# Kernel tuning notes

Measured on AMD Instinct MI355X. Metric: run time of the kernel, lower is better.

Reference implementation:

```python
import jax, jax.numpy as jnp
import numpy as np

N = 100000      # nodes
E = 1600000     # directed edges
F_IN = 128      # node feature dim
H = 128         # hidden dim
C = 16          # classes


def setup_inputs() -> dict:
    key = jax.random.key(0)
    ks = jax.random.split(key, 8)
    s = 1.0 / np.sqrt(H)
    return {
        "x": jax.random.normal(ks[0], (N, F_IN), dtype=jnp.float32),
        "edge_index": jax.random.randint(ks[1], (2, E), 0, N, dtype=jnp.int32),
        "W1": jax.random.normal(ks[2], (F_IN, H), dtype=jnp.float32) * s,
        "b1": jnp.zeros((H,), jnp.float32),
        "W2": jax.random.normal(ks[3], (H, H), dtype=jnp.float32) * s,
        "b2": jnp.zeros((H,), jnp.float32),
        "W3": jax.random.normal(ks[4], (H, H), dtype=jnp.float32) * s,
        "b3": jnp.zeros((H,), jnp.float32),
        "Wfc": jax.random.normal(ks[5], (H, C), dtype=jnp.float32) * s,
        "bfc": jnp.zeros((C,), jnp.float32),
    }


def _gcn_conv(x, W, b, src, dst, norm):
    # x' = b + scatter_add over edges of norm * (x @ W)[src] into dst
    h = x @ W                                   # [N, H] dense GEMM
    msg = h[src] * norm[:, None]                # [E+N, H] gather + scale
    out = jax.ops.segment_sum(msg, dst, num_segments=N)  # scatter-add
    return out + b


def reference(x, edge_index, W1, b1, W2, b2, W3, b3, Wfc, bfc):
    loops = jnp.arange(N, dtype=edge_index.dtype)
    src = jnp.concatenate([edge_index[0], loops])   # [E+N] with self-loops
    dst = jnp.concatenate([edge_index[1], loops])
    # symmetric normalization deg^{-1/2}[src] * deg^{-1/2}[dst] (PyG default)
    deg = jax.ops.segment_sum(jnp.ones_like(dst, dtype=x.dtype), dst, num_segments=N)
    dinv = jax.lax.rsqrt(deg)                       # deg >= 1 due to self-loops
    norm = dinv[src] * dinv[dst]

    h = jax.nn.elu(_gcn_conv(x, W1, b1, src, dst, norm))   # dropout is identity in eval
    h = jax.nn.elu(_gcn_conv(h, W2, b2, src, dst, norm))
    h = jax.nn.elu(_gcn_conv(h, W3, b3, src, dst, norm))
    logits = h @ Wfc + bfc                                  # [N, C]
    return jax.nn.log_softmax(logits, axis=-1)
```

## Files before the change

### kernel.cpp

```cpp
#include <hip/hip_runtime.h>
#include <math.h>

#define HDIM 128
#define CDIM 16
#define CAP 48
#define ASTR 136
#define NBINS 256
#define TILE 4096
#define F2SPLIT 4

typedef unsigned short u16;
typedef unsigned int u32;
typedef __attribute__((ext_vector_type(8))) short short8;
typedef __attribute__((ext_vector_type(4))) float f32x4;
typedef __attribute__((ext_vector_type(2))) float f32x2;

__device__ inline u16 f2bf(float f) {
  u32 u = __float_as_uint(f);
  u += 0x7fffu + ((u >> 16) & 1u);
  return (u16)(u >> 16);
}
__device__ inline float bf_lo(u32 p) { return __uint_as_float(p << 16); }
__device__ inline float bf_hi(u32 p) { return __uint_as_float(p & 0xffff0000u); }
__device__ inline u32 pack2(float a, float b) {
  return (u32)f2bf(a) | ((u32)f2bf(b) << 16);
}

__device__ inline void acc_word(f32x2& acc, u32 w) {
  f32x2 x;
  x.x = __uint_as_float(w << 16);
  x.y = __uint_as_float(w & 0xffff0000u);
  asm("v_pk_add_f32 %0, %1, %2" : "=v"(acc) : "v"(x), "v"(acc));
}
__device__ inline f32x2 xor16_add(f32x2 a) {
  f32x2 o;
  o.x = __shfl_xor(a.x, 16, 32);
  o.y = __shfl_xor(a.y, 16, 32);
  asm("v_pk_add_f32 %0, %1, %2" : "=v"(a) : "v"(o), "v"(a));
  return a;
}


__global__ __launch_bounds__(256) void bin_kernel(const int* __restrict__ ei,
                                                  int* __restrict__ cursor,
                                                  int2* __restrict__ bins,
                                                  int binCap, int E, int npb, int nbE,
                                                  int* __restrict__ deg, int N,
                                                  const float* __restrict__ W0,
                                                  const float* __restrict__ W1,
                                                  const float* __restrict__ W2,
                                                  u16* __restrict__ Wt) {
  int tid = threadIdx.x;
  if (blockIdx.x >= nbE) {
    int t = (blockIdx.x - nbE) * 256 + tid;
    int which = t >> 14, idx = t & 16383;
    int n = idx >> 7, k = idx & 127;
    const float* W = which == 0 ? W0 : (which == 1 ? W1 : W2);
    Wt[(size_t)which * HDIM * HDIM + n * HDIM + k] = f2bf(W[k * HDIM + n]);
    return;
  }
  {
    int i = blockIdx.x * 256 + tid;
    if (i < N) deg[i] = 0;
  }
  __shared__ int2 eds[TILE];
  __shared__ int base[NBINS], rank[NBINS], hist[NBINS];
  int t0 = blockIdx.x * TILE;
  int n = min(TILE, E - t0);
  for (int i = tid; i < NBINS; i += 256) { hist[i] = 0; rank[i] = 0; }
  __syncthreads();
  for (int i = tid; i < n; i += 256) {
    int s = ei[t0 + i];
    int d = ei[E + t0 + i];
    eds[i] = make_int2(d, s);
    atomicAdd(&hist[d / npb], 1);
  }
  __syncthreads();
  for (int i = tid; i < NBINS; i += 256) {
    int h = hist[i];
    base[i] = h ? atomicAdd(&cursor[i], h) : 0;
  }
  __syncthreads();
  for (int i = tid; i < n; i += 256) {
    int2 e = eds[i];
    int b = e.x / npb;
    int r = base[b] + atomicAdd(&rank[b], 1);
    if (r < binCap) bins[(size_t)b * binCap + r] = e;
  }
}

__global__ __launch_bounds__(256) void fill2_kernel(const int2* __restrict__ bins,
                                                    const int* __restrict__ cursor,
                                                    int binCap, int* __restrict__ deg,
                                                    int* __restrict__ csr) {
  int b = blockIdx.x & (NBINS - 1);
  int part = blockIdx.x >> 8;
  int cnt = min(cursor[b], binCap);
  const int2* eb = bins + (size_t)b * binCap;
  for (int i = part * 256 + threadIdx.x; i < cnt; i += 256 * F2SPLIT) {
    int2 e = eb[i];
    int p = atomicAdd(&deg[e.x], 1);
    if (p < CAP) csr[(size_t)e.x * CAP + p] = e.y;
  }
}

__global__ __launch_bounds__(256) void pad_kernel(const int* __restrict__ deg,
                                                  int* __restrict__ csr, int N) {
  int n = blockIdx.x * 256 + threadIdx.x;
  if (n >= N) return;
  int d = min(deg[n], CAP);
  int dp = (d + 15) & ~15;
  int* row = csr + (size_t)n * CAP;
  for (int i = d; i < dp; ++i) row[i] = N;
}


template <bool FP32IN>
__global__ __launch_bounds__(256) void gemm_k(const void* __restrict__ Xv,
                                              const u16* __restrict__ Wt,
                                              const int* __restrict__ deg,
                                              u16* __restrict__ G, int N) {
  __shared__ u16 As[64 * ASTR];
  __shared__ u16 Wsm[128 * ASTR];
  int tid = threadIdx.x;
  int row0 = blockIdx.x * 64;

  {
    int r = tid >> 2, c = tid & 3;
    int rg = row0 + r;
    if (rg >= N) rg = N - 1;
    uint4* dst = (uint4*)(As + r * ASTR + c * 32);
    if (FP32IN) {
      const float4* src = (const float4*)((const float*)Xv + (size_t)rg * HDIM + c * 32);
#pragma unroll
      for (int j = 0; j < 4; ++j) {
        float4 a = src[2 * j], b = src[2 * j + 1];
        uint4 o;
        o.x = pack2(a.x, a.y); o.y = pack2(a.z, a.w);
        o.z = pack2(b.x, b.y); o.w = pack2(b.z, b.w);
        dst[j] = o;
      }
    } else {
      const uint4* src = (const uint4*)((const u16*)Xv + (size_t)rg * HDIM + c * 32);
      dst[0] = src[0]; dst[1] = src[1]; dst[2] = src[2]; dst[3] = src[3];
    }
  }
  {
    int r = tid >> 1, h = tid & 1;
    const uint4* src = (const uint4*)(Wt + r * HDIM + h * 64);
    uint4* dst = (uint4*)(Wsm + r * ASTR + h * 64);
#pragma unroll
    for (int i = 0; i < 8; ++i) dst[i] = src[i];
  }
  __syncthreads();

  int w = tid >> 6;
  int l = tid & 63;
  int m = l & 15, q = l >> 4;

  f32x4 acc[8];
#pragma unroll
  for (int i = 0; i < 8; ++i) acc[i] = (f32x4){0.f, 0.f, 0.f, 0.f};

#pragma unroll
  for (int kc = 0; kc < 4; ++kc) {
    short8 af = *(const short8*)(As + (w * 16 + m) * ASTR + kc * 32 + q * 8);
#pragma unroll
    for (int nt = 0; nt < 8; ++nt) {
      short8 bfr = *(const short8*)(Wsm + (nt * 16 + m) * ASTR + kc * 32 + q * 8);
      acc[nt] = __builtin_amdgcn_mfma_f32_16x16x32_bf16(af, bfr, acc[nt], 0, 0, 0);
    }
  }
  __syncthreads();

  float dv[4];
#pragma unroll
  for (int r = 0; r < 4; ++r) {
    int rg = row0 + w * 16 + q * 4 + r;
    dv[r] = rsqrtf((float)(deg[rg < N ? rg : N - 1] + 1));
  }
#pragma unroll
  for (int nt = 0; nt < 8; ++nt)
#pragma unroll
    for (int r = 0; r < 4; ++r)
      As[(w * 16 + q * 4 + r) * ASTR + nt * 16 + m] = f2bf(acc[nt][r] * dv[r]);
  __syncthreads();

  {
    int r = tid >> 2, c = tid & 3;
    int rg = row0 + r;
    if (rg < N) {
      uint4* dst = (uint4*)(G + (size_t)rg * HDIM + c * 32);
      const uint4* src = (const uint4*)(As + r * ASTR + c * 32);
      dst[0] = src[0]; dst[1] = src[1]; dst[2] = src[2]; dst[3] = src[3];
    }
  }
}


__device__ inline void gather32(const u16* __restrict__ G, const int* __restrict__ deg,
                                const int* __restrict__ csr,
                                const float4* __restrict__ b4, int node, int cl, float* v) {
  const char* Gb = (const char*)G;
  int l = cl & 15, g = cl >> 4;
  uint4 sr = make_uint4(0, 0, 0, 0);
  if (g == 0) sr = *(const uint4*)(Gb + ((size_t)node << 8) + (l << 4));
  f32x2 p0, p1, p2, p3;
  p0.x = bf_lo(sr.x); p0.y = bf_hi(sr.x);
  p1.x = bf_lo(sr.y); p1.y = bf_hi(sr.y);
  p2.x = bf_lo(sr.z); p2.y = bf_hi(sr.z);
  p3.x = bf_lo(sr.w); p3.y = bf_hi(sr.w);

  int dfull = deg[node];
  int d = min(dfull, CAP);
  int dp = (d + 15) & ~15;
  const int* row = csr + (size_t)node * CAP;
  int i0 = row[cl];
  int i1 = (cl < 16) ? row[32 + cl] : 0;

#define GLD(u) (*(const uint4*)(Gb + (((u32)(u)) << 8) + (l << 4)))
#define AW(gv) { acc_word(p0, gv.x); acc_word(p1, gv.y); acc_word(p2, gv.z); acc_word(p3, gv.w); }
  for (int k = 0; k < dp; k += 16) {
    int s = k < 32 ? i0 : i1;
    int bl = (k < 32 ? k : 0) + g;
    int u0 = __shfl(s, bl + 0, 32), u1 = __shfl(s, bl + 2, 32);
    int u2 = __shfl(s, bl + 4, 32), u3 = __shfl(s, bl + 6, 32);
    int u4 = __shfl(s, bl + 8, 32), u5 = __shfl(s, bl + 10, 32);
    int u6 = __shfl(s, bl + 12, 32), u7 = __shfl(s, bl + 14, 32);
    uint4 g0 = GLD(u0), g1 = GLD(u1), g2 = GLD(u2), g3 = GLD(u3);
    uint4 g4 = GLD(u4), g5 = GLD(u5), g6 = GLD(u6), g7 = GLD(u7);
    AW(g0) AW(g1) AW(g2) AW(g3) AW(g4) AW(g5) AW(g6) AW(g7)
  }
#undef AW
#undef GLD
  p0 = xor16_add(p0); p1 = xor16_add(p1);
  p2 = xor16_add(p2); p3 = xor16_add(p3);

  float dvn = rsqrtf((float)(dfull + 1));
  float4 b0 = b4[l * 2], b1 = b4[l * 2 + 1];
  v[0] = fmaf(dvn, p0.x, b0.x); v[1] = fmaf(dvn, p0.y, b0.y);
  v[2] = fmaf(dvn, p1.x, b0.z); v[3] = fmaf(dvn, p1.y, b0.w);
  v[4] = fmaf(dvn, p2.x, b1.x); v[5] = fmaf(dvn, p2.y, b1.y);
  v[6] = fmaf(dvn, p3.x, b1.z); v[7] = fmaf(dvn, p3.y, b1.w);
#pragma unroll
  for (int j = 0; j < 8; ++j) v[j] = v[j] > 0.f ? v[j] : expm1f(v[j]);
}


__global__ __launch_bounds__(256) void agg_bf(const u16* __restrict__ G,
                                              const int* __restrict__ deg,
                                              const int* __restrict__ csr,
                                              const float* __restrict__ b,
                                              u16* __restrict__ out, int N) {
  int node = blockIdx.x * 8 + (threadIdx.x >> 5);
  if (node >= N) return;
  int cl = threadIdx.x & 31;
  float v[8];
  gather32(G, deg, csr, (const float4*)b, node, cl, v);
  if (cl < 16) {
    uint4 o;
    o.x = pack2(v[0], v[1]); o.y = pack2(v[2], v[3]);
    o.z = pack2(v[4], v[5]); o.w = pack2(v[6], v[7]);
    *(uint4*)(out + (size_t)node * HDIM + cl * 8) = o;
  }
}


__global__ __launch_bounds__(256) void agg_fc(const u16* __restrict__ G,
                                              const int* __restrict__ deg,
                                              const int* __restrict__ csr,
                                              const float* __restrict__ b,
                                              const float* __restrict__ Wfc,
                                              const float* __restrict__ bfc,
                                              float* __restrict__ out, int N) {
  __shared__ u16 As[8 * ASTR];
  __shared__ float Wl[HDIM * CDIM];
  int tid = threadIdx.x;
  for (int i = tid; i < HDIM * CDIM; i += 256) Wl[i] = Wfc[i];

  int node0 = blockIdx.x * 8;
  int nr = tid >> 5, cl = tid & 31, l = cl & 15;
  int node = node0 + nr;
  if (node < N) {
    float v[8];
    gather32(G, deg, csr, (const float4*)b, node, cl, v);
    if (cl < 16) {
      uint4 o;
      o.x = pack2(v[0], v[1]); o.y = pack2(v[2], v[3]);
      o.z = pack2(v[4], v[5]); o.w = pack2(v[6], v[7]);
      *(uint4*)(As + nr * ASTR + l * 8) = o;
    }
  }
  __syncthreads();

  int lr = tid >> 4, c = tid & 15;
  if (lr >= 8) return;
  int rg = node0 + lr;
  if (rg >= N) return;
  const u16* hrow = As + lr * ASTR;
  float acc = bfc[c];
#pragma unroll 4
  for (int k8 = 0; k8 < 16; ++k8) {
    uint4 g = *(const uint4*)(hrow + k8 * 8);
    const float* wk = Wl + (k8 * 8) * CDIM + c;
    acc = fmaf(bf_lo(g.x), wk[0 * CDIM], acc);
    acc = fmaf(bf_hi(g.x), wk[1 * CDIM], acc);
    acc = fmaf(bf_lo(g.y), wk[2 * CDIM], acc);
    acc = fmaf(bf_hi(g.y), wk[3 * CDIM], acc);
    acc = fmaf(bf_lo(g.z), wk[4 * CDIM], acc);
    acc = fmaf(bf_hi(g.z), wk[5 * CDIM], acc);
    acc = fmaf(bf_lo(g.w), wk[6 * CDIM], acc);
    acc = fmaf(bf_hi(g.w), wk[7 * CDIM], acc);
  }
  float mx = acc;
  for (int off = 8; off >= 1; off >>= 1) mx = fmaxf(mx, __shfl_xor(mx, off, 16));
  float ex = expf(acc - mx);
  float ssum = ex;
  for (int off = 8; off >= 1; off >>= 1) ssum += __shfl_xor(ssum, off, 16);
  out[(size_t)rg * CDIM + c] = (acc - mx) - logf(ssum);
}


extern "C" void kernel_launch(void* const* d_in, const int* in_sizes, int n_in,
                              void* d_out, int out_size, void* d_ws, size_t ws_size,
                              hipStream_t stream) {
  const float* x   = (const float*)d_in[0];
  const int*   ei  = (const int*)d_in[1];
  const float* W1  = (const float*)d_in[2];
  const float* b1  = (const float*)d_in[3];
  const float* W2  = (const float*)d_in[4];
  const float* b2  = (const float*)d_in[5];
  const float* W3  = (const float*)d_in[6];
  const float* b3  = (const float*)d_in[7];
  const float* Wfc = (const float*)d_in[8];
  const float* bfc = (const float*)d_in[9];

  const int N = in_sizes[0] / HDIM;
  const int E = in_sizes[1] / 2;
  const int npb = (N + NBINS - 1) / NBINS;
  const int binCap = (E + NBINS - 1) / NBINS + 1024;
  const int nbE = (E + TILE - 1) / TILE;
  const int nbW = 3 * HDIM * HDIM / 256;

  char* ws = (char*)d_ws;
  size_t off = 0;
  auto alloc = [&](size_t bytes) -> void* {
    void* p = ws + off;
    off += (bytes + 511) & ~(size_t)511;
    return p;
  };
  int*   deg    = (int*)alloc((size_t)N * 4);
  int*   cursor = (int*)alloc((size_t)NBINS * 4);
  int*   csr    = (int*)alloc((size_t)N * CAP * 4);
  int2*  bins   = (int2*)alloc((size_t)NBINS * binCap * 8);
  u16*   Wt     = (u16*)alloc((size_t)3 * HDIM * HDIM * 2);
  u16*   A      = (u16*)alloc((size_t)(N + 1) * HDIM * 2);
  u16*   B      = (u16*)alloc((size_t)(N + 1) * HDIM * 2);

  hipMemsetAsync(cursor, 0, (size_t)NBINS * 4, stream);
  hipMemsetAsync(A + (size_t)N * HDIM, 0, HDIM * 2, stream);
  hipMemsetAsync(B + (size_t)N * HDIM, 0, HDIM * 2, stream);
  bin_kernel<<<nbE + nbW, 256, 0, stream>>>(ei, cursor, bins, binCap, E, npb, nbE, deg, N, W1,
                                            W2, W3, Wt);
  fill2_kernel<<<NBINS * F2SPLIT, 256, 0, stream>>>(bins, cursor, binCap, deg, csr);
  pad_kernel<<<(N + 255) / 256, 256, 0, stream>>>(deg, csr, N);

  int grid64 = (N + 63) / 64;
  int grid8 = (N + 7) / 8;
  gemm_k<true><<<grid64, 256, 0, stream>>>(x, Wt, deg, A, N);
  agg_bf<<<grid8, 256, 0, stream>>>(A, deg, csr, b1, B, N);
  gemm_k<false><<<grid64, 256, 0, stream>>>(B, Wt + HDIM * HDIM, deg, A, N);
  agg_bf<<<grid8, 256, 0, stream>>>(A, deg, csr, b2, B, N);
  gemm_k<false><<<grid64, 256, 0, stream>>>(B, Wt + 2 * HDIM * HDIM, deg, A, N);
  agg_fc<<<grid8, 256, 0, stream>>>(A, deg, csr, b3, Wfc, bfc, (float*)d_out, N);
}
```

Measured before the change: 411.4 us.

## Aggregate each node with 16 lanes instead of 32 and drop cross-half reduction

The neighbour gather now assigns 16 lanes per node instead of 32 (two half-groups). Each lane walks all neighbours in steps of 8 with padding to multiples of 8, which removes the xor-shuffle reduction and the idle half-wave on writes. Other changes: 16 nodes per block, a hardware bf16 pack instruction, fast exp/log intrinsics, and the final FC reading fp32 hidden values from shared memory. Each lane now carries a longer serial dependent chain of loads per node, which may reduce memory-level parallelism per node, though more nodes are in flight per wave.

```diff
diff --git a/kernel.cpp b/kernel.cpp
--- a/kernel.cpp
+++ b/kernel.cpp
@@ -5,6 +5,7 @@
 #define CDIM 16
 #define CAP 48
 #define ASTR 136
+#define HSTR 132
 #define NBINS 256
 #define TILE 4096
 #define F2SPLIT 4
@@ -25,19 +26,16 @@
 __device__ inline u32 pack2(float a, float b) {
   return (u32)f2bf(a) | ((u32)f2bf(b) << 16);
 }
-
+__device__ inline u32 cvtpk(float a, float b) {
+  u32 r;
+  asm("v_cvt_pk_bf16_f32 %0, %1, %2" : "=v"(r) : "v"(a), "v"(b));
+  return r;
+}
 __device__ inline void acc_word(f32x2& acc, u32 w) {
   f32x2 x;
   x.x = __uint_as_float(w << 16);
   x.y = __uint_as_float(w & 0xffff0000u);
   asm("v_pk_add_f32 %0, %1, %2" : "=v"(acc) : "v"(x), "v"(acc));
-}
-__device__ inline f32x2 xor16_add(f32x2 a) {
-  f32x2 o;
-  o.x = __shfl_xor(a.x, 16, 32);
-  o.y = __shfl_xor(a.y, 16, 32);
-  asm("v_pk_add_f32 %0, %1, %2" : "=v"(a) : "v"(o), "v"(a));
-  return a;
 }
 
 
@@ -109,7 +107,7 @@
   int n = blockIdx.x * 256 + threadIdx.x;
   if (n >= N) return;
   int d = min(deg[n], CAP);
-  int dp = (d + 15) & ~15;
+  int dp = (d + 7) & ~7;
   int* row = csr + (size_t)n * CAP;
   for (int i = d; i < dp; ++i) row[i] = N;
 }
@@ -198,44 +196,41 @@
 }
 
 
-__device__ inline void gather32(const u16* __restrict__ G, const int* __restrict__ deg,
+__device__ inline void gather16(const u16* __restrict__ G, const int* __restrict__ deg,
                                 const int* __restrict__ csr,
-                                const float4* __restrict__ b4, int node, int cl, float* v) {
+                                const float4* __restrict__ b4, int node, int l, float* v) {
   const char* Gb = (const char*)G;
-  int l = cl & 15, g = cl >> 4;
-  uint4 sr = make_uint4(0, 0, 0, 0);
-  if (g == 0) sr = *(const uint4*)(Gb + ((size_t)node << 8) + (l << 4));
   f32x2 p0, p1, p2, p3;
-  p0.x = bf_lo(sr.x); p0.y = bf_hi(sr.x);
-  p1.x = bf_lo(sr.y); p1.y = bf_hi(sr.y);
-  p2.x = bf_lo(sr.z); p2.y = bf_hi(sr.z);
-  p3.x = bf_lo(sr.w); p3.y = bf_hi(sr.w);
-
+  {
+    uint4 sr = *(const uint4*)(Gb + ((size_t)node << 8) + (l << 4));
+    p0.x = bf_lo(sr.x); p0.y = bf_hi(sr.x);
+    p1.x = bf_lo(sr.y); p1.y = bf_hi(sr.y);
+    p2.x = bf_lo(sr.z); p2.y = bf_hi(sr.z);
+    p3.x = bf_lo(sr.w); p3.y = bf_hi(sr.w);
+  }
   int dfull = deg[node];
   int d = min(dfull, CAP);
-  int dp = (d + 15) & ~15;
+  int dp = (d + 7) & ~7;
   const int* row = csr + (size_t)node * CAP;
-  int i0 = row[cl];
-  int i1 = (cl < 16) ? row[32 + cl] : 0;
+  int i0 = row[l];
+  int i1 = d > 16 ? row[16 + l] : 0;
+  int i2 = d > 32 ? row[32 + l] : 0;
 
 #define GLD(u) (*(const uint4*)(Gb + (((u32)(u)) << 8) + (l << 4)))
 #define AW(gv) { acc_word(p0, gv.x); acc_word(p1, gv.y); acc_word(p2, gv.z); acc_word(p3, gv.w); }
-  for (int k = 0; k < dp; k += 16) {
-    int s = k < 32 ? i0 : i1;
-    int bl = (k < 32 ? k : 0) + g;
-    int u0 = __shfl(s, bl + 0, 32), u1 = __shfl(s, bl + 2, 32);
-    int u2 = __shfl(s, bl + 4, 32), u3 = __shfl(s, bl + 6, 32);
-    int u4 = __shfl(s, bl + 8, 32), u5 = __shfl(s, bl + 10, 32);
-    int u6 = __shfl(s, bl + 12, 32), u7 = __shfl(s, bl + 14, 32);
+  for (int k = 0; k < dp; k += 8) {
+    int s = k < 16 ? i0 : (k < 32 ? i1 : i2);
+    int bl = k & 15;
+    int u0 = __shfl(s, bl + 0, 16), u1 = __shfl(s, bl + 1, 16);
+    int u2 = __shfl(s, bl + 2, 16), u3 = __shfl(s, bl + 3, 16);
+    int u4 = __shfl(s, bl + 4, 16), u5 = __shfl(s, bl + 5, 16);
+    int u6 = __shfl(s, bl + 6, 16), u7 = __shfl(s, bl + 7, 16);
     uint4 g0 = GLD(u0), g1 = GLD(u1), g2 = GLD(u2), g3 = GLD(u3);
     uint4 g4 = GLD(u4), g5 = GLD(u5), g6 = GLD(u6), g7 = GLD(u7);
     AW(g0) AW(g1) AW(g2) AW(g3) AW(g4) AW(g5) AW(g6) AW(g7)
   }
 #undef AW
 #undef GLD
-  p0 = xor16_add(p0); p1 = xor16_add(p1);
-  p2 = xor16_add(p2); p3 = xor16_add(p3);
-
   float dvn = rsqrtf((float)(dfull + 1));
   float4 b0 = b4[l * 2], b1 = b4[l * 2 + 1];
   v[0] = fmaf(dvn, p0.x, b0.x); v[1] = fmaf(dvn, p0.y, b0.y);
@@ -243,7 +238,7 @@
   v[4] = fmaf(dvn, p2.x, b1.x); v[5] = fmaf(dvn, p2.y, b1.y);
   v[6] = fmaf(dvn, p3.x, b1.z); v[7] = fmaf(dvn, p3.y, b1.w);
 #pragma unroll
-  for (int j = 0; j < 8; ++j) v[j] = v[j] > 0.f ? v[j] : expm1f(v[j]);
+  for (int j = 0; j < 8; ++j) v[j] = v[j] > 0.f ? v[j] : __expf(v[j]) - 1.f;
 }
 
 
@@ -252,17 +247,15 @@
                                               const int* __restrict__ csr,
                                               const float* __restrict__ b,
                                               u16* __restrict__ out, int N) {
-  int node = blockIdx.x * 8 + (threadIdx.x >> 5);
+  int node = blockIdx.x * 16 + (threadIdx.x >> 4);
   if (node >= N) return;
-  int cl = threadIdx.x & 31;
+  int l = threadIdx.x & 15;
   float v[8];
-  gather32(G, deg, csr, (const float4*)b, node, cl, v);
-  if (cl < 16) {
-    uint4 o;
-    o.x = pack2(v[0], v[1]); o.y = pack2(v[2], v[3]);
-    o.z = pack2(v[4], v[5]); o.w = pack2(v[6], v[7]);
-    *(uint4*)(out + (size_t)node * HDIM + cl * 8) = o;
-  }
+  gather16(G, deg, csr, (const float4*)b, node, l, v);
+  uint4 o;
+  o.x = cvtpk(v[0], v[1]); o.y = cvtpk(v[2], v[3]);
+  o.z = cvtpk(v[4], v[5]); o.w = cvtpk(v[6], v[7]);
+  *(uint4*)(out + (size_t)node * HDIM + l * 8) = o;
 }
 
 
@@ -273,51 +266,43 @@
                                               const float* __restrict__ Wfc,
                                               const float* __restrict__ bfc,
                                               float* __restrict__ out, int N) {
-  __shared__ u16 As[8 * ASTR];
+  __shared__ float Hs[16 * HSTR];
   __shared__ float Wl[HDIM * CDIM];
   int tid = threadIdx.x;
   for (int i = tid; i < HDIM * CDIM; i += 256) Wl[i] = Wfc[i];
 
-  int node0 = blockIdx.x * 8;
-  int nr = tid >> 5, cl = tid & 31, l = cl & 15;
-  int node = node0 + nr;
+  int node0 = blockIdx.x * 16;
+  int lr = tid >> 4, l = tid & 15;
+  int node = node0 + lr;
   if (node < N) {
     float v[8];
-    gather32(G, deg, csr, (const float4*)b, node, cl, v);
-    if (cl < 16) {
-      uint4 o;
-      o.x = pack2(v[0], v[1]); o.y = pack2(v[2], v[3]);
-      o.z = pack2(v[4], v[5]); o.w = pack2(v[6], v[7]);
-      *(uint4*)(As + nr * ASTR + l * 8) = o;
-    }
-  }
-  __syncthreads();
-
-  int lr = tid >> 4, c = tid & 15;
-  if (lr >= 8) return;
+    gather16(G, deg, csr, (const float4*)b, node, l, v);
+    float4* dst = (float4*)(Hs + lr * HSTR + l * 8);
+    dst[0] = make_float4(v[0], v[1], v[2], v[3]);
+    dst[1] = make_float4(v[4], v[5], v[6], v[7]);
+  }
+  __syncthreads();
+
   int rg = node0 + lr;
   if (rg >= N) return;
-  const u16* hrow = As + lr * ASTR;
+  int c = l;
+  const float* hrow = Hs + lr * HSTR;
   float acc = bfc[c];
 #pragma unroll 4
-  for (int k8 = 0; k8 < 16; ++k8) {
-    uint4 g = *(const uint4*)(hrow + k8 * 8);
-    const float* wk = Wl + (k8 * 8) * CDIM + c;
-    acc = fmaf(bf_lo(g.x), wk[0 * CDIM], acc);
-    acc = fmaf(bf_hi(g.x), wk[1 * CDIM], acc);
-    acc = fmaf(bf_lo(g.y), wk[2 * CDIM], acc);
-    acc = fmaf(bf_hi(g.y), wk[3 * CDIM], acc);
-    acc = fmaf(bf_lo(g.z), wk[4 * CDIM], acc);
-    acc = fmaf(bf_hi(g.z), wk[5 * CDIM], acc);
-    acc = fmaf(bf_lo(g.w), wk[6 * CDIM], acc);
-    acc = fmaf(bf_hi(g.w), wk[7 * CDIM], acc);
+  for (int k4 = 0; k4 < 32; ++k4) {
+    float4 g = *(const float4*)(hrow + k4 * 4);
+    const float* wk = Wl + (k4 * 4) * CDIM + c;
+    acc = fmaf(g.x, wk[0 * CDIM], acc);
+    acc = fmaf(g.y, wk[1 * CDIM], acc);
+    acc = fmaf(g.z, wk[2 * CDIM], acc);
+    acc = fmaf(g.w, wk[3 * CDIM], acc);
   }
   float mx = acc;
   for (int off = 8; off >= 1; off >>= 1) mx = fmaxf(mx, __shfl_xor(mx, off, 16));
-  float ex = expf(acc - mx);
+  float ex = __expf(acc - mx);
   float ssum = ex;
   for (int off = 8; off >= 1; off >>= 1) ssum += __shfl_xor(ssum, off, 16);
-  out[(size_t)rg * CDIM + c] = (acc - mx) - logf(ssum);
+  out[(size_t)rg * CDIM + c] = (acc - mx) - __logf(ssum);
 }
 
 
@@ -366,11 +351,11 @@
   pad_kernel<<<(N + 255) / 256, 256, 0, stream>>>(deg, csr, N);
 
   int grid64 = (N + 63) / 64;
-  int grid8 = (N + 7) / 8;
+  int grid16 = (N + 15) / 16;
   gemm_k<true><<<grid64, 256, 0, stream>>>(x, Wt, deg, A, N);
-  agg_bf<<<grid8, 256, 0, stream>>>(A, deg, csr, b1, B, N);
+  agg_bf<<<grid16, 256, 0, stream>>>(A, deg, csr, b1, B, N);
   gemm_k<false><<<grid64, 256, 0, stream>>>(B, Wt + HDIM * HDIM, deg, A, N);
-  agg_bf<<<grid8, 256, 0, stream>>>(A, deg, csr, b2, B, N);
+  agg_bf<<<grid16, 256, 0, stream>>>(A, deg, csr, b2, B, N);
   gemm_k<false><<<grid64, 256, 0, stream>>>(B, Wt + 2 * HDIM * HDIM, deg, A, N);
-  agg_fc<<<grid8, 256, 0, stream>>>(A, deg, csr, b3, Wfc, bfc, (float*)d_out, N);
-}
+  agg_fc<<<grid16, 256, 0, stream>>>(A, deg, csr, b3, Wfc, bfc, (float*)d_out, N);
+}
```

Measured after the change: 406.9 us. About the same (-1.1%).
